# Kernel tuning notes

Measured on AMD Instinct MI355X. Metric: run time of the kernel, lower is better.

Reference implementation:

```python
import jax, jax.numpy as jnp
import numpy as np

N_NODES = 50000
N_EDGES = 800000
C = 128
NEG_SLOPE = 0.01  # nn.LeakyReLU default


def _init_linear(key, fan_in, fan_out):
    kw, kb = jax.random.split(key)
    lim = 1.0 / np.sqrt(fan_in)
    W = jax.random.uniform(kw, (fan_in, fan_out), jnp.float32, -lim, lim)
    b = jax.random.uniform(kb, (fan_out,), jnp.float32, -lim, lim)
    return W, b


def setup_inputs() -> dict:
    key = jax.random.key(0)
    ks = jax.random.split(key, 10)
    x = jax.random.normal(ks[0], (N_NODES, C), jnp.float32)
    pos = jax.random.normal(ks[1], (N_NODES, 3), jnp.float32)
    edge_index = jax.random.randint(ks[2], (2, N_EDGES), 0, N_NODES, jnp.int64)
    # mlp_h: Linear(C,C) -> LeakyReLU -> Linear(C,3) -> Tanh
    Wh1, bh1 = _init_linear(ks[3], C, C)
    Wh2, bh2 = _init_linear(ks[4], C, 3)
    # mlp_f: Linear(C+3, C) -> LeakyReLU
    Wf, bf = _init_linear(ks[5], C + 3, C)
    # mlp_g: Linear(C,C) -> LeakyReLU -> Linear(C,C)
    Wg1, bg1 = _init_linear(ks[6], C, C)
    Wg2, bg2 = _init_linear(ks[7], C, C)
    return {"x": x, "pos": pos, "edge_index": edge_index,
            "Wh1": Wh1, "bh1": bh1, "Wh2": Wh2, "bh2": bh2,
            "Wf": Wf, "bf": bf,
            "Wg1": Wg1, "bg1": bg1, "Wg2": Wg2, "bg2": bg2}


def reference(x, pos, edge_index, Wh1, bh1, Wh2, bh2, Wf, bf, Wg1, bg1, Wg2, bg2):
    lrelu = lambda t: jax.nn.leaky_relu(t, NEG_SLOPE)
    # delta_i = tanh(mlp_h(x_i))  -> [N, 3]
    delta = jnp.tanh(lrelu(x @ Wh1 + bh1) @ Wh2 + bh2)
    src, dst = edge_index[0], edge_index[1]  # message j -> i (PyG convention)
    # per-edge relative position: pos_j - pos_i + delta_i  -> [E, 3]
    rel = pos[src] - pos[dst] + delta[dst]
    # per-edge message: mlp_f([rel, x_j])  -> [E, C]
    e = lrelu(jnp.concatenate([rel, x[src]], axis=-1) @ Wf + bf)
    # scatter-max aggregate over incoming edges per target node
    agg = jax.ops.segment_max(e, dst, num_segments=N_NODES)
    agg = jnp.where(jnp.isfinite(agg), agg, 0.0)  # empty segments -> 0
    # out_i = mlp_g(agg_i) + x_i
    out = lrelu(agg @ Wg1 + bg1) @ Wg2 + bg2 + x
    return out
```

## Files before the change

kernel.cpp:

```cpp
#include <hip/hip_runtime.h>
#include <cfloat>
#include <cmath>

#define NEG_SLOPE 0.01f

typedef __attribute__((ext_vector_type(8))) short short8;
typedef __attribute__((ext_vector_type(4))) float f32x4;

__device__ __forceinline__ float lrelu(float v) { return v >= 0.0f ? v : NEG_SLOPE * v; }

__device__ __forceinline__ ushort f2b(float f) {
    unsigned u = __float_as_uint(f);
    u += 0x7fffu + ((u >> 16) & 1u);
    return (ushort)(u >> 16);
}
__device__ __forceinline__ float b2f(ushort s) { return __uint_as_float(((unsigned)s) << 16); }

__device__ __forceinline__ void split8(const float* v, short8& hi, short8& lo) {
#pragma unroll
    for (int j = 0; j < 8; ++j) {
        ushort h = f2b(v[j]);
        hi[j] = (short)h;
        lo[j] = (short)f2b(v[j] - b2f(h));
    }
}

__global__ __launch_bounds__(256) void wprep_kernel(
    const float* __restrict__ Wh1, const float* __restrict__ Wf,
    const float* __restrict__ Wg1, const float* __restrict__ Wg2,
    ushort* __restrict__ WT)
{
    int tt = blockIdx.x * 256 + threadIdx.x;
    int mat = tt >> 14;
    int idx = tt & 16383;
    int n = idx >> 7, k = idx & 127;
    float v;
    if (mat == 0)      v = Wh1[k * 128 + n];
    else if (mat == 1) v = Wf[(k + 3) * 128 + n];
    else if (mat == 2) v = Wg1[k * 128 + n];
    else               v = Wg2[k * 128 + n];
    WT[(tt - idx) + n * 128 + k] = f2b(v);
}

__global__ __launch_bounds__(256) void scan_partition_kernel(
    const int* __restrict__ ei, const int* __restrict__ G,
    int* __restrict__ bbase, uint* __restrict__ bpairs, int E)
{
    __shared__ int s[256];
    __shared__ int cur[256];
    const int b = blockIdx.x;
    const int t = threadIdx.x;

    int cs = 0, pp = 0;
    for (int bb = 0; bb < 256; ++bb) {
        int v = G[bb * 256 + t];
        if (bb < b) pp += v;
        cs += v;
    }
    s[t] = cs;
    __syncthreads();
    for (int d = 1; d < 256; d <<= 1) {
        int a = (t >= d) ? s[t - d] : 0;
        __syncthreads();
        s[t] += a;
        __syncthreads();
    }
    int colbase = s[t] - cs;
    cur[t] = colbase + pp;
    if (b == 0) {
        bbase[t] = colbase;
        if (t == 255) bbase[256] = colbase + cs;
    }
    __syncthreads();

    for (int e = b * 256 + t; e < E; e += 65536) {
        int src = ei[e];
        int dst = ei[E + e];
        int p = atomicAdd(&cur[dst >> 8], 1);
        bpairs[p] = (uint)src | ((uint)(dst & 255) << 24);
    }
}

__global__ __launch_bounds__(256) void bucket_csr_kernel(
    const uint* __restrict__ bpairs, const int* __restrict__ bbase,
    int* __restrict__ offs, int* __restrict__ srcs, int E, int M, int NBK)
{
    __shared__ int deg[256], scn[256], cur[256];
    const int b = blockIdx.x;
    const int t = threadIdx.x;
    const int base = bbase[b];
    const int end  = bbase[b + 1];
    deg[t] = 0;
    __syncthreads();
    for (int p = base + t; p < end; p += 256)
        atomicAdd(&deg[bpairs[p] >> 24], 1);
    __syncthreads();
    scn[t] = deg[t];
    __syncthreads();
    for (int d = 1; d < 256; d <<= 1) {
        int a = (t >= d) ? scn[t - d] : 0;
        __syncthreads();
        scn[t] += a;
        __syncthreads();
    }
    int excl = scn[t] - deg[t];
    cur[t] = excl;
    int node = b * 256 + t;
    if (node < M) offs[node] = base + excl;
    if (node == M - 1 || (b == NBK - 1 && t == 255)) offs[M] = E;
    __syncthreads();
    for (int p = base + t; p < end; p += 256) {
        uint pk = bpairs[p];
        int qpos = atomicAdd(&cur[pk >> 24], 1);
        srcs[base + qpos] = (int)(pk & 0xFFFFFFu);
    }
}


#define GEMM_CORE_REG(ACC, AH, AL)                                              \
    {                                                                           \
        _Pragma("unroll")                                                       \
        for (int ks = 0; ks < 4; ++ks) {                                        \
            _Pragma("unroll")                                                   \
            for (int nt = 0; nt < 8; ++nt) {                                    \
                short8 bfr = *(const short8*)&Bs[(nt * 16 + ln) * 136 + ks * 32 + qd * 8]; \
                ACC[nt] = __builtin_amdgcn_mfma_f32_16x16x32_bf16(AL[ks], bfr, ACC[nt], 0, 0, 0); \
                ACC[nt] = __builtin_amdgcn_mfma_f32_16x16x32_bf16(AH[ks], bfr, ACC[nt], 0, 0, 0); \
            }                                                                   \
        }                                                                       \
    }

#define STAGE_B(WTP)                                                            \
    {                                                                           \
        _Pragma("unroll")                                                       \
        for (int i = 0; i < 8; ++i) {                                           \
            int c = tid + 256 * i;                                              \
            int r = c >> 4, col8 = (c & 15) * 8;                                \
            *(uint4*)&Bs[r * 136 + col8] = *(const uint4*)((WTP) + r * 128 + col8); \
        }                                                                       \
    }

__global__ __launch_bounds__(256) void fused_count_hy_kernel(
    const int* __restrict__ ei, int* __restrict__ G, int E,
    const float* __restrict__ x, const ushort* __restrict__ WT,
    const float* __restrict__ bh1, const float* __restrict__ Wh2,
    const float* __restrict__ bh2, const float* __restrict__ Wf,
    const float* __restrict__ pos, float* __restrict__ q,
    ushort* __restrict__ yb, int M)
{
    __shared__ ushort Bs[128 * 136];
    __shared__ ushort yS[64 * 128];
    const int tid = threadIdx.x;

    if (blockIdx.x < 256) {
        int* cnt = (int*)yS;
        const int b = blockIdx.x;
        cnt[tid] = 0;
        __syncthreads();
        for (int e = b * 256 + tid; e < E; e += 65536)
            atomicAdd(&cnt[ei[E + e] >> 8], 1);
        __syncthreads();
        G[b * 256 + tid] = cnt[tid];
        return;
    }

    const int w = tid >> 6, L = tid & 63, qd = L >> 4, ln = L & 15;
    const int row0 = (blockIdx.x - 256) * 64;
    const int arow = row0 + w * 16 + ln;

    short8 ah[4], al[4];
    {
        const float* base = x + (size_t)((arow < M) ? arow : 0) * 128 + qd * 8;
        float vb[8];
#pragma unroll
        for (int ks = 0; ks < 4; ++ks) {
            float4 v0 = make_float4(0.f, 0.f, 0.f, 0.f), v1 = v0;
            if (arow < M) {
                v0 = *(const float4*)(base + ks * 32);
                v1 = *(const float4*)(base + ks * 32 + 4);
            }
            vb[0] = v0.x; vb[1] = v0.y; vb[2] = v0.z; vb[3] = v0.w;
            vb[4] = v1.x; vb[5] = v1.y; vb[6] = v1.z; vb[7] = v1.w;
            split8(vb, ah[ks], al[ks]);
        }
    }

    STAGE_B(WT);
    __syncthreads();
    f32x4 acc1[8];
#pragma unroll
    for (int nt = 0; nt < 8; ++nt) acc1[nt] = (f32x4){0.f, 0.f, 0.f, 0.f};
    GEMM_CORE_REG(acc1, ah, al);
    __syncthreads();

    STAGE_B(WT + 16384);
    __syncthreads();
    f32x4 acc2[8];
#pragma unroll
    for (int nt = 0; nt < 8; ++nt) acc2[nt] = (f32x4){0.f, 0.f, 0.f, 0.f};
    GEMM_CORE_REG(acc2, ah, al);
    __syncthreads();

    float* h1s = (float*)Bs;
#pragma unroll
    for (int nt = 0; nt < 8; ++nt) {
        int n = nt * 16 + ln;
        float bias = bh1[n];
#pragma unroll
        for (int r = 0; r < 4; ++r)
            h1s[(w * 16 + qd * 4 + r) * 132 + n] = lrelu(acc1[nt][r] + bias);
    }
#pragma unroll
    for (int r = 0; r < 4; ++r) {
        int m = w * 16 + qd * 4 + r;
        int gm = row0 + m;
        float p0 = 0.f, p1 = 0.f, p2 = 0.f;
        if (gm < M) { p0 = pos[gm * 3]; p1 = pos[gm * 3 + 1]; p2 = pos[gm * 3 + 2]; }
#pragma unroll
        for (int nt = 0; nt < 8; ++nt) {
            int n = nt * 16 + ln;
            yS[m * 128 + n] = f2b(acc2[nt][r] + p0 * Wf[n] + p1 * Wf[128 + n] + p2 * Wf[256 + n]);
        }
    }
    __syncthreads();

    int row = tid & 63, cc = tid >> 6;
    if (cc < 3 && row0 + row < M) {
        float s = 0.f;
#pragma unroll
        for (int k4 = 0; k4 < 32; ++k4) {
            float4 h = *(const float4*)&h1s[row * 132 + k4 * 4];
            s += h.x * Wh2[(k4 * 4 + 0) * 3 + cc] + h.y * Wh2[(k4 * 4 + 1) * 3 + cc]
               + h.z * Wh2[(k4 * 4 + 2) * 3 + cc] + h.w * Wh2[(k4 * 4 + 3) * 3 + cc];
        }
        q[(row0 + row) * 3 + cc] = tanhf(s + bh2[cc]) - pos[(row0 + row) * 3 + cc];
    }
#pragma unroll
    for (int i = 0; i < 4; ++i) {
        int c = tid + 256 * i;
        int r = c >> 4, col8 = (c & 15) * 8;
        if (row0 + r < M)
            *(uint4*)(yb + (size_t)(row0 + r) * 128 + col8) = *(const uint4*)&yS[r * 128 + col8];
    }
}

__global__ __launch_bounds__(256) void agg_kernel(
    const int* __restrict__ offs, const int* __restrict__ srcs,
    const ushort* __restrict__ yb, ushort* __restrict__ aggb, int M)
{
    int wave = threadIdx.x >> 6;
    int lane = threadIdx.x & 63;
    int node = blockIdx.x * 4 + wave;
    if (node >= M) return;
    int o0 = offs[node], o1 = offs[node + 1];
    float a0 = -INFINITY, a1 = -INFINITY;
    const uint* yp = (const uint*)yb;
    int j = o0;
    for (; j + 7 < o1; j += 8) {
        uint u[8];
#pragma unroll
        for (int t = 0; t < 8; ++t)
            u[t] = yp[(size_t)srcs[j + t] * 64 + lane];
#pragma unroll
        for (int t = 0; t < 8; ++t) {
            a0 = fmaxf(a0, __uint_as_float(u[t] << 16));
            a1 = fmaxf(a1, __uint_as_float(u[t] & 0xFFFF0000u));
        }
    }
    for (; j + 3 < o1; j += 4) {
        uint u[4];
#pragma unroll
        for (int t = 0; t < 4; ++t)
            u[t] = yp[(size_t)srcs[j + t] * 64 + lane];
#pragma unroll
        for (int t = 0; t < 4; ++t) {
            a0 = fmaxf(a0, __uint_as_float(u[t] << 16));
            a1 = fmaxf(a1, __uint_as_float(u[t] & 0xFFFF0000u));
        }
    }
    for (; j < o1; ++j) {
        uint u = yp[(size_t)srcs[j] * 64 + lane];
        a0 = fmaxf(a0, __uint_as_float(u << 16));
        a1 = fmaxf(a1, __uint_as_float(u & 0xFFFF0000u));
    }
    uint pk = (__float_as_uint(a0) >> 16) | (__float_as_uint(a1) & 0xFFFF0000u);
    ((uint*)aggb)[(size_t)node * 64 + lane] = pk;
}

__global__ __launch_bounds__(256) void midout_kernel(
    const ushort* __restrict__ aggb, const float* __restrict__ qv,
    const float* __restrict__ Wf, const float* __restrict__ bfv,
    const ushort* __restrict__ Wg1T, const float* __restrict__ bg1,
    const ushort* __restrict__ Wg2T, const float* __restrict__ bg2,
    const float* __restrict__ x, float* __restrict__ out, int M)
{
    __shared__ ushort Bs[128 * 136];
    __shared__ ushort Ms[64 * 136];
    const int tid = threadIdx.x;
    const int w = tid >> 6, L = tid & 63, qd = L >> 4, ln = L & 15;
    const int row0 = blockIdx.x * 64;
    const int arow = row0 + w * 16 + ln;

    short8 ah[4], al[4];
    {
        bool ok = arow < M;
        const ushort* base = aggb + (size_t)(ok ? arow : 0) * 128 + qd * 8;
        float q0 = 0.f, q1 = 0.f, q2 = 0.f;
        if (ok) { q0 = qv[arow * 3]; q1 = qv[arow * 3 + 1]; q2 = qv[arow * 3 + 2]; }
        float vb[8];
#pragma unroll
        for (int ks = 0; ks < 4; ++ks) {
            union { uint4 u; ushort s[8]; } a;
            a.u = ok ? *(const uint4*)(base + ks * 32) : make_uint4(0xFF80FF80u, 0xFF80FF80u, 0xFF80FF80u, 0xFF80FF80u);
#pragma unroll
            for (int j = 0; j < 8; ++j) {
                int k = ks * 32 + qd * 8 + j;
                float dec = 0.f;
                if (a.s[j] != 0xFF80u)
                    dec = lrelu(b2f(a.s[j]) + q0 * Wf[k] + q1 * Wf[128 + k] + q2 * Wf[256 + k] + bfv[k]);
                vb[j] = dec;
            }
            split8(vb, ah[ks], al[ks]);
        }
    }

    STAGE_B(Wg1T);
    __syncthreads();
    f32x4 macc[8];
#pragma unroll
    for (int nt = 0; nt < 8; ++nt) macc[nt] = (f32x4){0.f, 0.f, 0.f, 0.f};
    GEMM_CORE_REG(macc, ah, al);
    __syncthreads();

#pragma unroll
    for (int nt = 0; nt < 8; ++nt) {
        int n = nt * 16 + ln;
        float bias = bg1[n];
#pragma unroll
        for (int r = 0; r < 4; ++r)
            Ms[(w * 16 + qd * 4 + r) * 136 + n] = f2b(lrelu(macc[nt][r] + bias));
    }
    STAGE_B(Wg2T);
    __syncthreads();

    short8 a2[4];
#pragma unroll
    for (int ks = 0; ks < 4; ++ks)
        a2[ks] = *(const short8*)&Ms[(w * 16 + ln) * 136 + ks * 32 + qd * 8];

    f32x4 acc2[8];
#pragma unroll
    for (int nt = 0; nt < 8; ++nt) acc2[nt] = (f32x4){0.f, 0.f, 0.f, 0.f};
#pragma unroll
    for (int ks = 0; ks < 4; ++ks) {
#pragma unroll
        for (int nt = 0; nt < 8; ++nt) {
            short8 bfr = *(const short8*)&Bs[(nt * 16 + ln) * 136 + ks * 32 + qd * 8];
            acc2[nt] = __builtin_amdgcn_mfma_f32_16x16x32_bf16(a2[ks], bfr, acc2[nt], 0, 0, 0);
        }
    }
    __syncthreads();

    float* outS = (float*)Bs;
#pragma unroll
    for (int r = 0; r < 4; ++r) {
        int m = w * 16 + qd * 4 + r;
#pragma unroll
        for (int nt = 0; nt < 8; ++nt)
            outS[m * 132 + nt * 16 + ln] = acc2[nt][r];
    }
    __syncthreads();
#pragma unroll
    for (int i = 0; i < 8; ++i) {
        int c = tid + 256 * i;
        int r = c >> 5, col4 = (c & 31) * 4;
        int gr = row0 + r;
        if (gr < M) {
            float4 o = *(const float4*)&outS[r * 132 + col4];
            float4 bv = *(const float4*)(bg2 + col4);
            float4 xv = *(const float4*)(x + (size_t)gr * 128 + col4);
            o.x += bv.x + xv.x; o.y += bv.y + xv.y;
            o.z += bv.z + xv.z; o.w += bv.w + xv.w;
            *(float4*)(out + (size_t)gr * 128 + col4) = o;
        }
    }
}

extern "C" void kernel_launch(void* const* d_in, const int* in_sizes, int n_in,
                              void* d_out, int out_size, void* d_ws, size_t ws_size,
                              hipStream_t stream)
{
    const float* x   = (const float*)d_in[0];
    const float* pos = (const float*)d_in[1];
    const int*   ei  = (const int*)d_in[2];
    const float* Wh1 = (const float*)d_in[3];
    const float* bh1 = (const float*)d_in[4];
    const float* Wh2 = (const float*)d_in[5];
    const float* bh2 = (const float*)d_in[6];
    const float* Wf  = (const float*)d_in[7];
    const float* bf  = (const float*)d_in[8];
    const float* Wg1 = (const float*)d_in[9];
    const float* bg1 = (const float*)d_in[10];
    const float* Wg2 = (const float*)d_in[11];
    const float* bg2 = (const float*)d_in[12];
    float* out = (float*)d_out;

    const int M = in_sizes[0] / 128;
    const int E = in_sizes[2] / 2;
    const int NBK = (M + 255) >> 8;

    char* ws = (char*)d_ws;
    size_t off = 0;
    auto alloc = [&](size_t bytes) { void* p = ws + off; off += (bytes + 255) & ~255ull; return p; };
    ushort* yb     = (ushort*)alloc((size_t)M * 128 * sizeof(ushort));
    ushort* aggb   = (ushort*)alloc((size_t)M * 128 * sizeof(ushort));
    ushort* WT     = (ushort*)alloc(4 * 16384 * sizeof(ushort));
    float*  q      = (float*)alloc((size_t)M * 3 * sizeof(float));
    int*    offs   = (int*)alloc((size_t)(M + 1) * sizeof(int));
    int*    G      = (int*)alloc(256 * 256 * sizeof(int));
    int*    bbase  = (int*)alloc(257 * sizeof(int));
    uint*   bpairs = (uint*)alloc((size_t)E * sizeof(uint));
    int*    srcs   = (int*)alloc((size_t)E * sizeof(int));

    const int gb = (M + 63) / 64;

    wprep_kernel<<<256, 256, 0, stream>>>(Wh1, Wf, Wg1, Wg2, WT);
    fused_count_hy_kernel<<<256 + gb, 256, 0, stream>>>(
        ei, G, E, x, WT, bh1, Wh2, bh2, Wf, pos, q, yb, M);
    scan_partition_kernel<<<256, 256, 0, stream>>>(ei, G, bbase, bpairs, E);
    bucket_csr_kernel<<<NBK, 256, 0, stream>>>(bpairs, bbase, offs, srcs, E, M, NBK);
    agg_kernel<<<(M + 3) / 4, 256, 0, stream>>>(offs, srcs, yb, aggb, M);
    midout_kernel<<<gb, 256, 0, stream>>>(aggb, q, Wf, bf,
                                          WT + 2 * 16384, bg1,
                                          WT + 3 * 16384, bg2, x, out, M);
}
```

Baseline: 216.8 us.

## Regroup kernels so edge counting runs with weight prep and scan-partition with the node GEMM

The destination-count histogram moves from the GEMM kernel into the weight-prep kernel, and the scan/partition step is merged into the GEMM kernel as 256 extra blocks. This cuts one launch and lets the edge partitioning overlap with the per-node MLP work instead of running in series after it. The scan blocks reuse the GEMM kernel's large shared-memory allocation, which may reduce how many of those blocks fit per CU.

```diff
diff --git a/kernel.cpp b/kernel.cpp
--- a/kernel.cpp
+++ b/kernel.cpp
@@ -25,95 +25,35 @@
     }
 }
 
-__global__ __launch_bounds__(256) void wprep_kernel(
+__global__ __launch_bounds__(256) void count_wprep_kernel(
+    const int* __restrict__ ei, int* __restrict__ G, int E,
     const float* __restrict__ Wh1, const float* __restrict__ Wf,
     const float* __restrict__ Wg1, const float* __restrict__ Wg2,
     ushort* __restrict__ WT)
 {
-    int tt = blockIdx.x * 256 + threadIdx.x;
-    int mat = tt >> 14;
-    int idx = tt & 16383;
-    int n = idx >> 7, k = idx & 127;
-    float v;
-    if (mat == 0)      v = Wh1[k * 128 + n];
-    else if (mat == 1) v = Wf[(k + 3) * 128 + n];
-    else if (mat == 2) v = Wg1[k * 128 + n];
-    else               v = Wg2[k * 128 + n];
-    WT[(tt - idx) + n * 128 + k] = f2b(v);
-}
-
-__global__ __launch_bounds__(256) void scan_partition_kernel(
-    const int* __restrict__ ei, const int* __restrict__ G,
-    int* __restrict__ bbase, uint* __restrict__ bpairs, int E)
-{
-    __shared__ int s[256];
-    __shared__ int cur[256];
+    __shared__ int cnt[256];
+    const int t = threadIdx.x;
     const int b = blockIdx.x;
-    const int t = threadIdx.x;
-
-    int cs = 0, pp = 0;
-    for (int bb = 0; bb < 256; ++bb) {
-        int v = G[bb * 256 + t];
-        if (bb < b) pp += v;
-        cs += v;
-    }
-    s[t] = cs;
-    __syncthreads();
-    for (int d = 1; d < 256; d <<= 1) {
-        int a = (t >= d) ? s[t - d] : 0;
-        __syncthreads();
-        s[t] += a;
-        __syncthreads();
-    }
-    int colbase = s[t] - cs;
-    cur[t] = colbase + pp;
-    if (b == 0) {
-        bbase[t] = colbase;
-        if (t == 255) bbase[256] = colbase + cs;
-    }
-    __syncthreads();
-
-    for (int e = b * 256 + t; e < E; e += 65536) {
-        int src = ei[e];
-        int dst = ei[E + e];
-        int p = atomicAdd(&cur[dst >> 8], 1);
-        bpairs[p] = (uint)src | ((uint)(dst & 255) << 24);
-    }
-}
-
-__global__ __launch_bounds__(256) void bucket_csr_kernel(
-    const uint* __restrict__ bpairs, const int* __restrict__ bbase,
-    int* __restrict__ offs, int* __restrict__ srcs, int E, int M, int NBK)
-{
-    __shared__ int deg[256], scn[256], cur[256];
-    const int b = blockIdx.x;
-    const int t = threadIdx.x;
-    const int base = bbase[b];
-    const int end  = bbase[b + 1];
-    deg[t] = 0;
-    __syncthreads();
-    for (int p = base + t; p < end; p += 256)
-        atomicAdd(&deg[bpairs[p] >> 24], 1);
-    __syncthreads();
-    scn[t] = deg[t];
-    __syncthreads();
-    for (int d = 1; d < 256; d <<= 1) {
-        int a = (t >= d) ? scn[t - d] : 0;
-        __syncthreads();
-        scn[t] += a;
-        __syncthreads();
-    }
-    int excl = scn[t] - deg[t];
-    cur[t] = excl;
-    int node = b * 256 + t;
-    if (node < M) offs[node] = base + excl;
-    if (node == M - 1 || (b == NBK - 1 && t == 255)) offs[M] = E;
-    __syncthreads();
-    for (int p = base + t; p < end; p += 256) {
-        uint pk = bpairs[p];
-        int qpos = atomicAdd(&cur[pk >> 24], 1);
-        srcs[base + qpos] = (int)(pk & 0xFFFFFFu);
-    }
+
+    {
+        int tt = b * 256 + t;
+        int mat = tt >> 14;
+        int idx = tt & 16383;
+        int n = idx >> 7, k = idx & 127;
+        float v;
+        if (mat == 0)      v = Wh1[k * 128 + n];
+        else if (mat == 1) v = Wf[(k + 3) * 128 + n];
+        else if (mat == 2) v = Wg1[k * 128 + n];
+        else               v = Wg2[k * 128 + n];
+        WT[(tt - idx) + n * 128 + k] = f2b(v);
+    }
+
+    cnt[t] = 0;
+    __syncthreads();
+    for (int e = b * 256 + t; e < E; e += 65536)
+        atomicAdd(&cnt[ei[E + e] >> 8], 1);
+    __syncthreads();
+    G[b * 256 + t] = cnt[t];
 }
 
 
@@ -140,8 +80,9 @@
         }                                                                       \
     }
 
-__global__ __launch_bounds__(256) void fused_count_hy_kernel(
-    const int* __restrict__ ei, int* __restrict__ G, int E,
+__global__ __launch_bounds__(256) void hy_scanpart_kernel(
+    const int* __restrict__ ei, const int* __restrict__ G,
+    int* __restrict__ bbase, uint* __restrict__ bpairs, int E, int GB,
     const float* __restrict__ x, const ushort* __restrict__ WT,
     const float* __restrict__ bh1, const float* __restrict__ Wh2,
     const float* __restrict__ bh2, const float* __restrict__ Wf,
@@ -152,20 +93,45 @@
     __shared__ ushort yS[64 * 128];
     const int tid = threadIdx.x;
 
-    if (blockIdx.x < 256) {
-        int* cnt = (int*)yS;
-        const int b = blockIdx.x;
-        cnt[tid] = 0;
+    if (blockIdx.x >= GB) {
+        int* s   = (int*)yS;
+        int* cur = ((int*)yS) + 256;
+        const int b = blockIdx.x - GB;
+        const int t = tid;
+
+        int cs = 0, pp = 0;
+        for (int bb = 0; bb < 256; ++bb) {
+            int v = G[bb * 256 + t];
+            if (bb < b) pp += v;
+            cs += v;
+        }
+        s[t] = cs;
         __syncthreads();
-        for (int e = b * 256 + tid; e < E; e += 65536)
-            atomicAdd(&cnt[ei[E + e] >> 8], 1);
+        for (int d = 1; d < 256; d <<= 1) {
+            int a = (t >= d) ? s[t - d] : 0;
+            __syncthreads();
+            s[t] += a;
+            __syncthreads();
+        }
+        int colbase = s[t] - cs;
+        cur[t] = colbase + pp;
+        if (b == 0) {
+            bbase[t] = colbase;
+            if (t == 255) bbase[256] = colbase + cs;
+        }
         __syncthreads();
-        G[b * 256 + tid] = cnt[tid];
+
+        for (int e = b * 256 + t; e < E; e += 65536) {
+            int src = ei[e];
+            int dst = ei[E + e];
+            int p = atomicAdd(&cur[dst >> 8], 1);
+            bpairs[p] = (uint)src | ((uint)(dst & 255) << 24);
+        }
         return;
     }
 
     const int w = tid >> 6, L = tid & 63, qd = L >> 4, ln = L & 15;
-    const int row0 = (blockIdx.x - 256) * 64;
+    const int row0 = blockIdx.x * 64;
     const int arow = row0 + w * 16 + ln;
 
     short8 ah[4], al[4];
@@ -241,6 +207,41 @@
         int r = c >> 4, col8 = (c & 15) * 8;
         if (row0 + r < M)
             *(uint4*)(yb + (size_t)(row0 + r) * 128 + col8) = *(const uint4*)&yS[r * 128 + col8];
+    }
+}
+
+__global__ __launch_bounds__(256) void bucket_csr_kernel(
+    const uint* __restrict__ bpairs, const int* __restrict__ bbase,
+    int* __restrict__ offs, int* __restrict__ srcs, int E, int M, int NBK)
+{
+    __shared__ int deg[256], scn[256], cur[256];
+    const int b = blockIdx.x;
+    const int t = threadIdx.x;
+    const int base = bbase[b];
+    const int end  = bbase[b + 1];
+    deg[t] = 0;
+    __syncthreads();
+    for (int p = base + t; p < end; p += 256)
+        atomicAdd(&deg[bpairs[p] >> 24], 1);
+    __syncthreads();
+    scn[t] = deg[t];
+    __syncthreads();
+    for (int d = 1; d < 256; d <<= 1) {
+        int a = (t >= d) ? scn[t - d] : 0;
+        __syncthreads();
+        scn[t] += a;
+        __syncthreads();
+    }
+    int excl = scn[t] - deg[t];
+    cur[t] = excl;
+    int node = b * 256 + t;
+    if (node < M) offs[node] = base + excl;
+    if (node == M - 1 || (b == NBK - 1 && t == 255)) offs[M] = E;
+    __syncthreads();
+    for (int p = base + t; p < end; p += 256) {
+        uint pk = bpairs[p];
+        int qpos = atomicAdd(&cur[pk >> 24], 1);
+        srcs[base + qpos] = (int)(pk & 0xFFFFFFu);
     }
 }
 
@@ -424,10 +425,10 @@
 
     const int gb = (M + 63) / 64;
 
-    wprep_kernel<<<256, 256, 0, stream>>>(Wh1, Wf, Wg1, Wg2, WT);
-    fused_count_hy_kernel<<<256 + gb, 256, 0, stream>>>(
-        ei, G, E, x, WT, bh1, Wh2, bh2, Wf, pos, q, yb, M);
-    scan_partition_kernel<<<256, 256, 0, stream>>>(ei, G, bbase, bpairs, E);
+    count_wprep_kernel<<<256, 256, 0, stream>>>(ei, G, E, Wh1, Wf, Wg1, Wg2, WT);
+    hy_scanpart_kernel<<<gb + 256, 256, 0, stream>>>(
+        ei, G, bbase, bpairs, E, gb,
+        x, WT, bh1, Wh2, bh2, Wf, pos, q, yb, M);
     bucket_csr_kernel<<<NBK, 256, 0, stream>>>(bpairs, bbase, offs, srcs, E, M, NBK);
     agg_kernel<<<(M + 3) / 4, 256, 0, stream>>>(offs, srcs, yb, aggb, M);
     midout_kernel<<<gb, 256, 0, stream>>>(aggb, q, Wf, bf,
```

New measurement: 208.2 us. 1.04x faster.
